# Kernel optimization log

Measured on AMD Instinct MI355X. Metric: run time of the kernel, lower is better.

Reference implementation:

```python
import jax, jax.numpy as jnp
import numpy as np

B, NQ, NK, D = 4, 512, 1024, 64
SCALE = 1.0


def _xavier(key, fan_in, fan_out):
    lim = np.sqrt(6.0 / (fan_in + fan_out))
    return jax.random.uniform(key, (fan_in, fan_out), jnp.float32, -lim, lim)


def setup_inputs() -> dict:
    key = jax.random.key(0)
    ks = jax.random.split(key, 7)
    return {
        "x1": jax.random.normal(ks[0], (B, NK, D), jnp.float32),   # context x -> keys
        "x2": jax.random.normal(ks[1], (B, NQ, D), jnp.float32),   # target x  -> queries
        "r":  jax.random.normal(ks[2], (B, NK, D), jnp.float32),   # values
        # key-path MLP (linear_layers_list): Linear(64,64) -> relu -> Linear(64,64)
        "Wk1": _xavier(ks[3], D, D), "bk1": jnp.zeros((D,), jnp.float32),
        "Wk2": _xavier(ks[4], D, D), "bk2": jnp.zeros((D,), jnp.float32),
        # query-path MLP (linear_layers_list2)
        "Wq1": _xavier(ks[5], D, D), "bq1": jnp.zeros((D,), jnp.float32),
        "Wq2": _xavier(ks[6], D, D), "bq2": jnp.zeros((D,), jnp.float32),
    }


def _mlp(x, W1, b1, W2, b2):
    # relu on all layers except the last (matches the torch loop)
    h = jax.nn.relu(jnp.einsum('bsd,de->bse', x, W1) + b1)
    return jnp.einsum('bsd,de->bse', h, W2) + b2


def reference(x1, x2, r, Wk1, bk1, Wk2, bk2, Wq1, bq1, Wq2, bq2):
    k = _mlp(x1, Wk1, bk1, Wk2, bk2)          # [B, NK, D]
    q = _mlp(x2, Wq1, bq1, Wq2, bq2)          # [B, NQ, D]
    # laplace attention: -sum_d |(k - q)/scale|, broadcast [B, NQ, NK, D]
    unnorm = -jnp.sum(jnp.abs((k[:, None, :, :] - q[:, :, None, :]) / SCALE), axis=-1)  # [B, NQ, NK]
    weights = jax.nn.softmax(unnorm, axis=2)  # normalise=True -> softmax over keys
    return jnp.einsum('bik,bkj->bij', weights, r)  # [B, NQ, D]
```

## Files before the change

kernel.cpp:

```cpp
#include <hip/hip_runtime.h>
#include <math.h>

#define BB 4
#define NQ 512
#define NK 1024
#define DH 64
#define TQ 8
#define NWAVE 8
#define KPW (NK / NWAVE)

__global__ __launch_bounds__(64) void mlp_kernel(
    const float* __restrict__ x1, const float* __restrict__ x2,
    const float* __restrict__ Wk1, const float* __restrict__ bk1,
    const float* __restrict__ Wk2, const float* __restrict__ bk2,
    const float* __restrict__ Wq1, const float* __restrict__ bq1,
    const float* __restrict__ Wq2, const float* __restrict__ bq2,
    float* __restrict__ kT, float* __restrict__ qT)
{
    const int row  = blockIdx.x;
    const int lane = threadIdx.x;
    const float *x, *W1, *b1, *W2, *b2;
    float* out;
    if (row < BB * NK) {
        const int b = row / NK, j = row % NK;
        x = x1 + row * DH;
        W1 = Wk1; b1 = bk1; W2 = Wk2; b2 = bk2;
        out = kT + (size_t)b * DH * NK + j;
    } else {
        const int rq = row - BB * NK;
        const int b = rq / NQ, i = rq % NQ;
        x = x2 + rq * DH;
        W1 = Wq1; b1 = bq1; W2 = Wq2; b2 = bq2;
        out = qT + (size_t)b * DH * NQ + i;
    }
    const int ostride = (row < BB * NK) ? NK : NQ;

    __shared__ float xs[DH];
    __shared__ float hs[DH];
    xs[lane] = x[lane];
    __syncthreads();
    float acc = b1[lane];
    #pragma unroll
    for (int d = 0; d < DH; ++d) acc = fmaf(xs[d], W1[d * DH + lane], acc);
    hs[lane] = fmaxf(acc, 0.0f);
    __syncthreads();
    float acc2 = b2[lane];
    #pragma unroll
    for (int d = 0; d < DH; ++d) acc2 = fmaf(hs[d], W2[d * DH + lane], acc2);
    out[lane * ostride] = acc2;
}

__global__ __launch_bounds__(512) void attn_kernel(
    const float* __restrict__ kT, const float* __restrict__ qT,
    const float* __restrict__ rmat, float* __restrict__ outp)
{
    __shared__ float p_s[TQ * NK];
    __shared__ float wmin_s[NWAVE * TQ];
    __shared__ float wsum_s[NWAVE * TQ];

    const int t    = threadIdx.x;
    const int lane = t & 63;
    const int wav  = __builtin_amdgcn_readfirstlane(t >> 6);

    const int b  = blockIdx.x / (NQ / TQ);
    const int i0 = (blockIdx.x % (NQ / TQ)) * TQ;

    const float* kTb = kT + (size_t)b * DH * NK;
    const float* qTb = qT + (size_t)b * DH * NQ;

    const int j0 = wav * KPW + 2 * lane;

    float s0[TQ], s1[TQ];
    #pragma unroll
    for (int i = 0; i < TQ; ++i) { s0[i] = 0.0f; s1[i] = 0.0f; }

    #pragma unroll 8
    for (int d = 0; d < DH; ++d) {
        const float2 kv = *(const float2*)&kTb[d * NK + j0];
        const float* qrow = qTb + d * NQ + i0;
        #pragma unroll
        for (int i = 0; i < TQ; ++i) {
            const float q = qrow[i];
            s0[i] += fabsf(kv.x - q);
            s1[i] += fabsf(kv.y - q);
        }
    }

    #pragma unroll
    for (int i = 0; i < TQ; ++i) {
        float m = fminf(s0[i], s1[i]);
        #pragma unroll
        for (int off = 32; off > 0; off >>= 1)
            m = fminf(m, __shfl_xor(m, off, 64));
        if (lane == 0) wmin_s[wav * TQ + i] = m;
    }
    __syncthreads();

    float M[TQ];
    #pragma unroll
    for (int i = 0; i < TQ; ++i) {
        float m = wmin_s[i];
        #pragma unroll
        for (int g = 1; g < NWAVE; ++g) m = fminf(m, wmin_s[g * TQ + i]);
        M[i] = m;
    }

    #pragma unroll
    for (int i = 0; i < TQ; ++i) {
        const float p0 = __expf(M[i] - s0[i]);
        const float p1 = __expf(M[i] - s1[i]);
        *(float2*)&p_s[i * NK + j0] = make_float2(p0, p1);
        float cs = p0 + p1;
        #pragma unroll
        for (int off = 32; off > 0; off >>= 1)
            cs += __shfl_xor(cs, off, 64);
        if (lane == 0) wsum_s[wav * TQ + i] = cs;
    }
    __syncthreads();

    float myl = 0.0f;
    #pragma unroll
    for (int g = 0; g < NWAVE; ++g) myl += wsum_s[g * TQ + wav];

    float O[TQ];
    #pragma unroll
    for (int i = 0; i < TQ; ++i) O[i] = 0.0f;

    const float* rb = rmat + ((size_t)b * NK + wav * KPW) * DH;
    for (int jj = 0; jj < KPW; jj += 4) {
        const float rv0 = rb[(jj + 0) * DH + lane];
        const float rv1 = rb[(jj + 1) * DH + lane];
        const float rv2 = rb[(jj + 2) * DH + lane];
        const float rv3 = rb[(jj + 3) * DH + lane];
        #pragma unroll
        for (int i = 0; i < TQ; ++i) {
            const float4 p4 = *(const float4*)&p_s[i * NK + wav * KPW + jj];
            O[i] = fmaf(p4.x, rv0, O[i]);
            O[i] = fmaf(p4.y, rv1, O[i]);
            O[i] = fmaf(p4.z, rv2, O[i]);
            O[i] = fmaf(p4.w, rv3, O[i]);
        }
    }
    __syncthreads();

    float* part = p_s;
    #pragma unroll
    for (int i = 0; i < TQ; ++i)
        part[(wav * TQ + i) * 64 + lane] = O[i];
    __syncthreads();

    float sum = 0.0f;
    #pragma unroll
    for (int g = 0; g < NWAVE; ++g)
        sum += part[(g * TQ + wav) * 64 + lane];
    outp[((size_t)b * NQ + i0 + wav) * DH + lane] = sum / myl;
}

extern "C" void kernel_launch(void* const* d_in, const int* in_sizes, int n_in,
                              void* d_out, int out_size, void* d_ws, size_t ws_size,
                              hipStream_t stream) {
    const float* x1  = (const float*)d_in[0];
    const float* x2  = (const float*)d_in[1];
    const float* r   = (const float*)d_in[2];
    const float* Wk1 = (const float*)d_in[3];
    const float* bk1 = (const float*)d_in[4];
    const float* Wk2 = (const float*)d_in[5];
    const float* bk2 = (const float*)d_in[6];
    const float* Wq1 = (const float*)d_in[7];
    const float* bq1 = (const float*)d_in[8];
    const float* Wq2 = (const float*)d_in[9];
    const float* bq2 = (const float*)d_in[10];
    float* out  = (float*)d_out;

    float* kT = (float*)d_ws;
    float* qT = kT + (size_t)BB * DH * NK;

    mlp_kernel<<<BB * (NK + NQ), 64, 0, stream>>>(
        x1, x2, Wk1, bk1, Wk2, bk2, Wq1, bq1, Wq2, bq2, kT, qT);

    attn_kernel<<<BB * (NQ / TQ), 512, 0, stream>>>(kT, qT, r, out);
}
```

Measured before the change: 108.3 us.

## Batch MLP rows per block with register-cached weights; retile attention to 4 queries

The MLP kernel now handles 16 rows per 256-thread block. Each lane keeps its W1/W2 columns in registers, and the hidden vector is broadcast with readlane instead of shared memory and barriers, which cuts the weight reloads and the launch of one tiny block per row. The attention kernel moves to 4 queries and 4 waves per block with float4 key loads, doubling the block count and halving shared memory so occupancy goes up. The cost is more register pressure (128 weight registers) and less reuse of each key load across queries.

```diff
diff --git a/kernel.cpp b/kernel.cpp
--- a/kernel.cpp
+++ b/kernel.cpp
@@ -5,11 +5,10 @@
 #define NQ 512
 #define NK 1024
 #define DH 64
-#define TQ 8
-#define NWAVE 8
-#define KPW (NK / NWAVE)
-
-__global__ __launch_bounds__(64) void mlp_kernel(
+
+#define MROWS 16
+
+__global__ __launch_bounds__(256, 2) void mlp_kernel(
     const float* __restrict__ x1, const float* __restrict__ x2,
     const float* __restrict__ Wk1, const float* __restrict__ bk1,
     const float* __restrict__ Wk2, const float* __restrict__ bk2,
@@ -17,40 +16,59 @@
     const float* __restrict__ Wq2, const float* __restrict__ bq2,
     float* __restrict__ kT, float* __restrict__ qT)
 {
-    const int row  = blockIdx.x;
-    const int lane = threadIdx.x;
-    const float *x, *W1, *b1, *W2, *b2;
-    float* out;
-    if (row < BB * NK) {
-        const int b = row / NK, j = row % NK;
-        x = x1 + row * DH;
-        W1 = Wk1; b1 = bk1; W2 = Wk2; b2 = bk2;
-        out = kT + (size_t)b * DH * NK + j;
-    } else {
-        const int rq = row - BB * NK;
-        const int b = rq / NQ, i = rq % NQ;
-        x = x2 + rq * DH;
-        W1 = Wq1; b1 = bq1; W2 = Wq2; b2 = bq2;
-        out = qT + (size_t)b * DH * NQ + i;
-    }
-    const int ostride = (row < BB * NK) ? NK : NQ;
-
-    __shared__ float xs[DH];
-    __shared__ float hs[DH];
-    xs[lane] = x[lane];
-    __syncthreads();
-    float acc = b1[lane];
-    #pragma unroll
-    for (int d = 0; d < DH; ++d) acc = fmaf(xs[d], W1[d * DH + lane], acc);
-    hs[lane] = fmaxf(acc, 0.0f);
-    __syncthreads();
-    float acc2 = b2[lane];
-    #pragma unroll
-    for (int d = 0; d < DH; ++d) acc2 = fmaf(hs[d], W2[d * DH + lane], acc2);
-    out[lane * ostride] = acc2;
+    const int t    = threadIdx.x;
+    const int lane = t & 63;
+    const int wav  = __builtin_amdgcn_readfirstlane(t >> 6);
+
+    const int  NKBLK = (BB * NK) / MROWS;
+    const bool isk   = (int)blockIdx.x < NKBLK;
+    const int  rblk  = isk ? (int)blockIdx.x : (int)blockIdx.x - NKBLK;
+
+    const float* __restrict__ xb = isk ? x1 : x2;
+    const float* __restrict__ W1 = isk ? Wk1 : Wq1;
+    const float* __restrict__ b1 = isk ? bk1 : bq1;
+    const float* __restrict__ W2 = isk ? Wk2 : Wq2;
+    const float* __restrict__ b2 = isk ? bk2 : bq2;
+    float* __restrict__ oT = isk ? kT : qT;
+    const int seq = isk ? NK : NQ;
+    const int lgs = isk ? 10 : 9;
+
+    float w1r[DH], w2r[DH];
+    #pragma unroll
+    for (int d = 0; d < DH; ++d) {
+        w1r[d] = W1[d * DH + lane];
+        w2r[d] = W2[d * DH + lane];
+    }
+    const float b1v = b1[lane];
+    const float b2v = b2[lane];
+
+    const int row0 = rblk * MROWS + wav * 4;
+    #pragma unroll
+    for (int rr = 0; rr < 4; ++rr) {
+        const int row = row0 + rr;
+        const float* xr = xb + (size_t)row * DH;
+        float acc = b1v;
+        #pragma unroll
+        for (int d = 0; d < DH; ++d) acc = fmaf(xr[d], w1r[d], acc);
+        const float h = fmaxf(acc, 0.0f);
+        float acc2 = b2v;
+        #pragma unroll
+        for (int d = 0; d < DH; ++d) {
+            const float hd = __int_as_float(
+                __builtin_amdgcn_readlane(__float_as_int(h), d));
+            acc2 = fmaf(hd, w2r[d], acc2);
+        }
+        const int bidx = row >> lgs;
+        const int sidx = row & (seq - 1);
+        oT[((size_t)bidx * DH + lane) * seq + sidx] = acc2;
+    }
 }
 
-__global__ __launch_bounds__(512) void attn_kernel(
+#define TQ 4
+#define NWAVE 4
+#define KPW (NK / NWAVE)
+
+__global__ __launch_bounds__(256, 2) void attn_kernel(
     const float* __restrict__ kT, const float* __restrict__ qT,
     const float* __restrict__ rmat, float* __restrict__ outp)
 {
@@ -68,27 +86,30 @@
     const float* kTb = kT + (size_t)b * DH * NK;
     const float* qTb = qT + (size_t)b * DH * NQ;
 
-    const int j0 = wav * KPW + 2 * lane;
-
-    float s0[TQ], s1[TQ];
-    #pragma unroll
-    for (int i = 0; i < TQ; ++i) { s0[i] = 0.0f; s1[i] = 0.0f; }
+    const int j0 = wav * KPW + 4 * lane;
+
+    float s[TQ][4];
+    #pragma unroll
+    for (int i = 0; i < TQ; ++i)
+        { s[i][0] = 0.f; s[i][1] = 0.f; s[i][2] = 0.f; s[i][3] = 0.f; }
 
     #pragma unroll 8
     for (int d = 0; d < DH; ++d) {
-        const float2 kv = *(const float2*)&kTb[d * NK + j0];
+        const float4 kv = *(const float4*)&kTb[d * NK + j0];
         const float* qrow = qTb + d * NQ + i0;
         #pragma unroll
         for (int i = 0; i < TQ; ++i) {
             const float q = qrow[i];
-            s0[i] += fabsf(kv.x - q);
-            s1[i] += fabsf(kv.y - q);
+            s[i][0] += fabsf(kv.x - q);
+            s[i][1] += fabsf(kv.y - q);
+            s[i][2] += fabsf(kv.z - q);
+            s[i][3] += fabsf(kv.w - q);
         }
     }
 
     #pragma unroll
     for (int i = 0; i < TQ; ++i) {
-        float m = fminf(s0[i], s1[i]);
+        float m = fminf(fminf(s[i][0], s[i][1]), fminf(s[i][2], s[i][3]));
         #pragma unroll
         for (int off = 32; off > 0; off >>= 1)
             m = fminf(m, __shfl_xor(m, off, 64));
@@ -107,10 +128,13 @@
 
     #pragma unroll
     for (int i = 0; i < TQ; ++i) {
-        const float p0 = __expf(M[i] - s0[i]);
-        const float p1 = __expf(M[i] - s1[i]);
-        *(float2*)&p_s[i * NK + j0] = make_float2(p0, p1);
-        float cs = p0 + p1;
+        float4 p4;
+        p4.x = __expf(M[i] - s[i][0]);
+        p4.y = __expf(M[i] - s[i][1]);
+        p4.z = __expf(M[i] - s[i][2]);
+        p4.w = __expf(M[i] - s[i][3]);
+        *(float4*)&p_s[i * NK + j0] = p4;
+        float cs = (p4.x + p4.y) + (p4.z + p4.w);
         #pragma unroll
         for (int off = 32; off > 0; off >>= 1)
             cs += __shfl_xor(cs, off, 64);
@@ -118,23 +142,19 @@
     }
     __syncthreads();
 
-    float myl = 0.0f;
-    #pragma unroll
-    for (int g = 0; g < NWAVE; ++g) myl += wsum_s[g * TQ + wav];
-
     float O[TQ];
     #pragma unroll
     for (int i = 0; i < TQ; ++i) O[i] = 0.0f;
 
     const float* rb = rmat + ((size_t)b * NK + wav * KPW) * DH;
-    for (int jj = 0; jj < KPW; jj += 4) {
-        const float rv0 = rb[(jj + 0) * DH + lane];
-        const float rv1 = rb[(jj + 1) * DH + lane];
-        const float rv2 = rb[(jj + 2) * DH + lane];
-        const float rv3 = rb[(jj + 3) * DH + lane];
+    for (int kk = 0; kk < KPW; kk += 4) {
+        const float rv0 = rb[(kk + 0) * DH + lane];
+        const float rv1 = rb[(kk + 1) * DH + lane];
+        const float rv2 = rb[(kk + 2) * DH + lane];
+        const float rv3 = rb[(kk + 3) * DH + lane];
         #pragma unroll
         for (int i = 0; i < TQ; ++i) {
-            const float4 p4 = *(const float4*)&p_s[i * NK + wav * KPW + jj];
+            const float4 p4 = *(const float4*)&p_s[i * NK + wav * KPW + kk];
             O[i] = fmaf(p4.x, rv0, O[i]);
             O[i] = fmaf(p4.y, rv1, O[i]);
             O[i] = fmaf(p4.z, rv2, O[i]);
@@ -149,11 +169,16 @@
         part[(wav * TQ + i) * 64 + lane] = O[i];
     __syncthreads();
 
+    const int q = wav;
     float sum = 0.0f;
     #pragma unroll
     for (int g = 0; g < NWAVE; ++g)
-        sum += part[(g * TQ + wav) * 64 + lane];
-    outp[((size_t)b * NQ + i0 + wav) * DH + lane] = sum / myl;
+        sum += part[(g * TQ + q) * 64 + lane];
+    float l = 0.0f;
+    #pragma unroll
+    for (int g = 0; g < NWAVE; ++g)
+        l += wsum_s[g * TQ + q];
+    outp[((size_t)b * NQ + i0 + q) * DH + lane] = sum / l;
 }
 
 extern "C" void kernel_launch(void* const* d_in, const int* in_sizes, int n_in,
@@ -170,13 +195,13 @@
     const float* bq1 = (const float*)d_in[8];
     const float* Wq2 = (const float*)d_in[9];
     const float* bq2 = (const float*)d_in[10];
-    float* out  = (float*)d_out;
+    float* out = (float*)d_out;
 
     float* kT = (float*)d_ws;
     float* qT = kT + (size_t)BB * DH * NK;
 
-    mlp_kernel<<<BB * (NK + NQ), 64, 0, stream>>>(
+    mlp_kernel<<<(BB * (NK + NQ)) / MROWS, 256, 0, stream>>>(
         x1, x2, Wk1, bk1, Wk2, bk2, Wq1, bq1, Wq2, bq2, kT, qT);
 
-    attn_kernel<<<BB * (NQ / TQ), 512, 0, stream>>>(kT, qT, r, out);
+    attn_kernel<<<BB * (NQ / TQ), 256, 0, stream>>>(kT, qT, r, out);
 }
```

Result: no change. 108.8 us (+0.5%).
